# Kernel optimization log

Hardware: AMD Instinct MI355X
Metric: run time of the kernel (lower is better)

The kernel has to match this reference:

```python
import jax, jax.numpy as jnp
import numpy as np

N_HEAD = 8

def setup_inputs() -> dict:
    key = jax.random.key(0)
    ks = jax.random.split(key, 5)
    N, C, T, V = 64, 128, 64, 25
    x = jax.random.normal(ks[0], (N, C, T, V), dtype=jnp.float32)
    Wa = jax.random.normal(ks[1], (C, C), dtype=jnp.float32) * (1.0 / np.sqrt(C))
    ba = jax.random.normal(ks[2], (C,), dtype=jnp.float32) * 0.01
    Wp = jax.random.normal(ks[3], (C, C), dtype=jnp.float32) * (1.0 / np.sqrt(C))
    bp = jax.random.normal(ks[4], (C,), dtype=jnp.float32) * 0.01
    temp = jnp.ones((N_HEAD, 1), dtype=jnp.float32)
    denom_bias = jnp.zeros((N_HEAD, 1, 1), dtype=jnp.float32)
    return {"x": x, "Wa": Wa, "ba": ba, "Wp": Wp, "bp": bp, "temp": temp, "denom_bias": denom_bias}

def reference(x, Wa, ba, Wp, bp, temp, denom_bias):
    # x: (N, C, T, V); eval mode (dropout = identity); residual = identity (in==out, stride==1)
    N, C, T, V = x.shape
    H = N_HEAD
    hd = C // H
    res = x
    # 1x1 conv c_attn
    w = jnp.einsum('nctv,oc->notv', x, Wa) + ba[None, :, None, None]
    # (N,H,hd,T,V) -> (N,H,T,V,hd) -> (N,H,T*V,hd)
    w = w.reshape(N, H, hd, T, V).transpose(0, 1, 3, 4, 2).reshape(N, H, T * V, hd)
    w_sq = w * w
    denom = jnp.maximum(jnp.cumsum(w_sq, axis=2), 1e-12)
    w_normed = w_sq / denom + denom_bias  # denom_bias (H,1,1) broadcasts
    tmp = jnp.sum(w_normed, axis=-1) * temp  # (N,H,L) * (H,1)
    Pi = jax.nn.softmax(tmp, axis=2)  # (N,H,L)
    dots = jnp.cumsum(w_sq * Pi[..., None], axis=2) / (jnp.cumsum(Pi, axis=2) + 1e-8)[..., None]
    attn = 1.0 / (1.0 + dots)
    y = -(w * Pi[..., None]) * attn  # (N,H,L,hd)
    y = y.reshape(N, H, T, V, hd).transpose(0, 1, 4, 2, 3).reshape(N, C, T, V)
    y = jnp.einsum('nctv,oc->notv', y, Wp) + bp[None, :, None, None]
    y = y + res
    return jax.nn.relu(y)
```

## Files before the change

kernel.cpp:

```cpp
#include <hip/hip_runtime.h>
#include <hip/hip_bf16.h>

#define N_S     64
#define C_CH    128
#define L_SEQ   1600
#define H_HEADS 8
#define HD      16
#define SEGN    32
#define SEGL    50
#define PADW    136
#define PADT    70
#define NHQ     12800

typedef __attribute__((ext_vector_type(8))) short bf16x8;
typedef __attribute__((ext_vector_type(4))) float f32x4;

__device__ inline unsigned short f2bf(float f) {
  return __builtin_bit_cast(unsigned short, __float2bfloat16(f));
}
__device__ inline float bflo(unsigned int u) { return __builtin_bit_cast(float, u << 16); }
__device__ inline float bfhi(unsigned int u) { return __builtin_bit_cast(float, u & 0xffff0000u); }
__device__ inline unsigned int pk(float a, float b) {
  return (unsigned int)f2bf(a) | ((unsigned int)f2bf(b) << 16);
}

template <int CTRL>
__device__ inline float dppadd(float x) {
  int r = __builtin_amdgcn_update_dpp(0, __builtin_bit_cast(int, x), CTRL, 0xF, 0xF, true);
  return x + __builtin_bit_cast(float, r);
}


__global__ __launch_bounds__(256) void k_gemm1(const float* __restrict__ x,
                                               const float* __restrict__ Wa,
                                               const float* __restrict__ ba,
                                               unsigned int* __restrict__ w3) {
  __shared__ unsigned short was[128 * PADW];
  __shared__ unsigned short xs[128 * PADT];
  const int n = blockIdx.y;
  const int l0 = blockIdx.x * 64;
  const int t = threadIdx.x;
  const float* xn = x + (size_t)n * (C_CH * L_SEQ);

#pragma unroll
  for (int it = 0; it < 16; ++it) {
    int pos = it * 256 + t;
    int o = pos >> 5;
    int c4 = (pos & 31) << 2;
    float4 v = *reinterpret_cast<const float4*>(Wa + o * C_CH + c4);
    ushort4 u;
    u.x = f2bf(v.x); u.y = f2bf(v.y); u.z = f2bf(v.z); u.w = f2bf(v.w);
    *reinterpret_cast<ushort4*>(&was[o * PADW + c4]) = u;
  }
#pragma unroll
  for (int it = 0; it < 8; ++it) {
    int pos = it * 256 + t;
    int c = pos >> 4;
    int l4 = (pos & 15) << 2;
    float4 v = *reinterpret_cast<const float4*>(xn + (size_t)c * L_SEQ + l0 + l4);
    ushort4 u;
    u.x = f2bf(v.x); u.y = f2bf(v.y); u.z = f2bf(v.z); u.w = f2bf(v.w);
    *reinterpret_cast<ushort4*>(&xs[c * PADT + l4]) = u;
  }
  __syncthreads();

  const int wv = t >> 6;
  const int lane = t & 63;
  const int r16 = lane & 15;
  const int kg = lane >> 4;
  f32x4 acc[8];
#pragma unroll
  for (int ot = 0; ot < 8; ++ot) acc[ot] = (f32x4){0.f, 0.f, 0.f, 0.f};

#pragma unroll
  for (int ks = 0; ks < 4; ++ks) {
    bf16x8 a;
#pragma unroll
    for (int j = 0; j < 8; ++j)
      a[j] = (short)xs[(ks * 32 + kg * 8 + j) * PADT + wv * 16 + r16];
#pragma unroll
    for (int ot = 0; ot < 8; ++ot) {
      bf16x8 b = *reinterpret_cast<const bf16x8*>(&was[(ot * 16 + r16) * PADW + ks * 32 + kg * 8]);
      acc[ot] = __builtin_amdgcn_mfma_f32_16x16x32_bf16(a, b, acc[ot], 0, 0, 0);
    }
  }
  const int lbase = l0 + wv * 16 + kg * 4;
  const unsigned int lp0 = (unsigned int)lbase >> 1;
  const unsigned int seg0 = lp0 / 25u;
  const unsigned int ii0 = lp0 - seg0 * 25u;
  const unsigned int seg1 = (ii0 == 24u) ? seg0 + 1u : seg0;
  const unsigned int ii1 = (ii0 == 24u) ? 0u : ii0 + 1u;
  const unsigned int off0 = ii0 * 512u + seg0 * 16u + (unsigned int)r16;
  const unsigned int off1 = ii1 * 512u + seg1 * 16u + (unsigned int)r16;
  unsigned int* w3n = w3 + (size_t)(n * H_HEADS) * NHQ;
#pragma unroll
  for (int ot = 0; ot < 8; ++ot) {
    float bav = ba[ot * 16 + r16];
    unsigned int* p = w3n + (size_t)ot * NHQ;
    p[off0] = pk(acc[ot][0] + bav, acc[ot][1] + bav);
    p[off1] = pk(acc[ot][2] + bav, acc[ot][3] + bav);
  }
}

__global__ __launch_bounds__(512) void k_scan(const unsigned int* __restrict__ w3,
                                              unsigned int* __restrict__ y3,
                                              const float* __restrict__ temp,
                                              const float* __restrict__ dbias) {
  __shared__ float stot[SEGN][17];
  __shared__ float red[8];

  const int nh = blockIdx.x;
  const int h = nh & 7;
  const int t = threadIdx.x;
  const int d = t & 15;
  const int lane = t & 63;
  const int wv = t >> 6;
  const int seg = t >> 4;
  const float tscale = temp[h];
  const float db16 = 16.f * dbias[h];
  const float M = fmaxf((16.f + db16) * tscale, db16 * tscale);

  unsigned int vp[25];
  const unsigned int* srcd = w3 + (size_t)nh * NHQ;
#pragma unroll
  for (int ii = 0; ii < 25; ++ii) vp[ii] = srcd[ii * 512 + t];

  float tot = 0.f;
#pragma unroll
  for (int ii = 0; ii < 25; ++ii) {
    float a = bflo(vp[ii]), b = bfhi(vp[ii]);
    tot += a * a + b * b;
  }
  stot[seg][d] = tot;
  __syncthreads();
#pragma unroll
  for (int it = 0; it < 2; ++it) {
    int col = wv + it * 8;
    float val = (lane < 32) ? stot[lane][col] : 0.f;
#pragma unroll
    for (int sh = 1; sh < 32; sh <<= 1) {
      float nv = __shfl_up(val, sh);
      if (lane >= sh) val += nv;
    }
    if (lane < 32) stot[lane][col] = val;
  }
  __syncthreads();
  const float off = stot[seg][d] - tot;

  unsigned int ep[25];
  float run = off;
  float sAcc = 0.f, wpAcc = 0.f;
  float eprev = 0.f;
#pragma unroll
  for (int i = 0; i < SEGL; ++i) {
    float v = (i & 1) ? bfhi(vp[i >> 1]) : bflo(vp[i >> 1]);
    float wsq = v * v;
    run += wsq;
    float c = __fdividef(wsq, fmaxf(run, 1e-12f));
    c = dppadd<0x128>(c);
    c = dppadd<0x124>(c);
    c = dppadd<0x122>(c);
    c = dppadd<0x121>(c);
    float e = __expf((c + db16) * tscale - M);
    sAcc += e;
    wpAcc = fmaf(wsq, e, wpAcc);
    if (i & 1) ep[i >> 1] = pk(eprev, e); else eprev = e;
  }
  {
    float s = sAcc;
#pragma unroll
    for (int mask = 32; mask; mask >>= 1) s += __shfl_xor(s, mask);
    if (lane == 0) red[wv] = s;
  }
  __syncthreads();
  float S16 = 0.f;
#pragma unroll
  for (int i2 = 0; i2 < 8; ++i2) S16 += red[i2];
  const float S = S16 * 0.0625f;
  const float ninvS = -1.0f / S;
  const float epsS = 1e-8f * S;

  stot[seg][d] = wpAcc;
  if (d == 0) stot[seg][16] = sAcc;
  __syncthreads();
#pragma unroll
  for (int it = 0; it < 2; ++it) {
    int col = wv + it * 8;
    float val = (lane < 32) ? stot[lane][col] : 0.f;
#pragma unroll
    for (int sh = 1; sh < 32; sh <<= 1) {
      float nv = __shfl_up(val, sh);
      if (lane >= sh) val += nv;
    }
    if (lane < 32) stot[lane][col] = val;
  }
  if (wv == 0) {
    float val = (lane < 32) ? stot[lane][16] : 0.f;
#pragma unroll
    for (int sh = 1; sh < 32; sh <<= 1) {
      float nv = __shfl_up(val, sh);
      if (lane >= sh) val += nv;
    }
    if (lane < 32) stot[lane][16] = val;
  }
  __syncthreads();
  const float wp_off = stot[seg][d] - wpAcc;
  const float pi_off = stot[seg][16] - sAcc;

  {
    float run_wp = wp_off, run_pi = pi_off;
    float ylo = 0.f;
#pragma unroll
    for (int i = 0; i < SEGL; ++i) {
      float v = (i & 1) ? bfhi(vp[i >> 1]) : bflo(vp[i >> 1]);
      float e = (i & 1) ? bfhi(ep[i >> 1]) : bflo(ep[i >> 1]);
      run_pi += e;
      run_wp = fmaf(v * v, e, run_wp);
      float dn = run_pi + epsS;
      float y = (v * e) * __fdividef(dn, dn + run_wp) * ninvS;
      if (i & 1) vp[i >> 1] = pk(ylo, y); else ylo = y;
    }
  }
  unsigned int* dstd = y3 + (size_t)nh * NHQ;
#pragma unroll
  for (int ii = 0; ii < 25; ++ii) dstd[ii * 512 + t] = vp[ii];
}

__global__ __launch_bounds__(256) void k_gemm2(const unsigned int* __restrict__ y3,
                                               const float* __restrict__ Wp,
                                               const float* __restrict__ bp,
                                               const float* __restrict__ x,
                                               float* __restrict__ out) {
  __shared__ unsigned short wps[128 * PADW];
  __shared__ unsigned short ys[128 * PADT];
  const int n = blockIdx.y;
  const int l0 = blockIdx.x * 64;
  const int t = threadIdx.x;

#pragma unroll
  for (int it = 0; it < 16; ++it) {
    int pos = it * 256 + t;
    int o = pos >> 5;
    int c4 = (pos & 31) << 2;
    float4 v = *reinterpret_cast<const float4*>(Wp + o * C_CH + c4);
    ushort4 u;
    u.x = f2bf(v.x); u.y = f2bf(v.y); u.z = f2bf(v.z); u.w = f2bf(v.w);
    *reinterpret_cast<ushort4*>(&wps[o * PADW + c4]) = u;
  }
  const int lpb = l0 >> 1;
#pragma unroll
  for (int k = 0; k < 16; ++k) {
    int e = k * 256 + t;
    int lpl = e >> 7;
    int hd = e & 127;
    unsigned int lp = (unsigned int)(lpb + lpl);
    unsigned int sg = lp / 25u;
    unsigned int ii = lp - sg * 25u;
    unsigned int vdw = y3[(size_t)(n * H_HEADS + (hd >> 4)) * NHQ + ii * 512u + sg * 16u + (hd & 15)];
    *reinterpret_cast<unsigned int*>(&ys[hd * PADT + 2 * lpl]) = vdw;
  }
  __syncthreads();

  const int wv = t >> 6;
  const int lane = t & 63;
  const int r16 = lane & 15;
  const int kg = lane >> 4;
  f32x4 acc[8];
#pragma unroll
  for (int ot = 0; ot < 8; ++ot) acc[ot] = (f32x4){0.f, 0.f, 0.f, 0.f};

#pragma unroll
  for (int ks = 0; ks < 4; ++ks) {
    bf16x8 b;
#pragma unroll
    for (int j = 0; j < 8; ++j)
      b[j] = (short)ys[(ks * 32 + kg * 8 + j) * PADT + wv * 16 + r16];
#pragma unroll
    for (int ot = 0; ot < 8; ++ot) {
      bf16x8 a = *reinterpret_cast<const bf16x8*>(&wps[(ot * 16 + r16) * PADW + ks * 32 + kg * 8]);
      acc[ot] = __builtin_amdgcn_mfma_f32_16x16x32_bf16(a, b, acc[ot], 0, 0, 0);
    }
  }
  const int gl = l0 + wv * 16 + r16;
#pragma unroll
  for (int ot = 0; ot < 8; ++ot) {
#pragma unroll
    for (int i = 0; i < 4; ++i) {
      int o = ot * 16 + kg * 4 + i;
      size_t idx = (size_t)n * (C_CH * L_SEQ) + (size_t)o * L_SEQ + gl;
      float r = acc[ot][i] + bp[o] + x[idx];
      out[idx] = fmaxf(r, 0.f);
    }
  }
}

extern "C" void kernel_launch(void* const* d_in, const int* in_sizes, int n_in,
                              void* d_out, int out_size, void* d_ws, size_t ws_size,
                              hipStream_t stream) {
  const float* x     = (const float*)d_in[0];
  const float* Wa    = (const float*)d_in[1];
  const float* ba    = (const float*)d_in[2];
  const float* Wp    = (const float*)d_in[3];
  const float* bp    = (const float*)d_in[4];
  const float* temp  = (const float*)d_in[5];
  const float* dbias = (const float*)d_in[6];
  float* out = (float*)d_out;

  unsigned int* w3 = (unsigned int*)d_ws;
  unsigned int* y3 = w3 + (size_t)N_S * H_HEADS * NHQ;

  k_gemm1<<<dim3(L_SEQ / 64, N_S), 256, 0, stream>>>(x, Wa, ba, w3);
  k_scan<<<N_S * H_HEADS, 512, 0, stream>>>(w3, y3, temp, dbias);
  k_gemm2<<<dim3(L_SEQ / 64, N_S), 256, 0, stream>>>(y3, Wp, bp, x, out);
}
```

Before: 74.70 us.

## Store scan output in channel-major layout for vectorized gemm2 loads

```diff
diff --git a/kernel.cpp b/kernel.cpp
--- a/kernel.cpp
+++ b/kernel.cpp
@@ -9,7 +9,7 @@
 #define SEGN    32
 #define SEGL    50
 #define PADW    136
-#define PADT    70
+#define PADT    72
 #define NHQ     12800
 
 typedef __attribute__((ext_vector_type(8))) short bf16x8;
@@ -103,7 +103,7 @@
 }
 
 __global__ __launch_bounds__(512) void k_scan(const unsigned int* __restrict__ w3,
-                                              unsigned int* __restrict__ y3,
+                                              unsigned short* __restrict__ y2,
                                               const float* __restrict__ temp,
                                               const float* __restrict__ dbias) {
   __shared__ float stot[SEGN][17];
@@ -119,6 +119,8 @@
   const float tscale = temp[h];
   const float db16 = 16.f * dbias[h];
   const float M = fmaxf((16.f + db16) * tscale, db16 * tscale);
+  const float A = tscale * 1.44269504088896f;
+  const float B = (db16 * tscale - M) * 1.44269504088896f;
 
   unsigned int vp[25];
   const unsigned int* srcd = w3 + (size_t)nh * NHQ;
@@ -161,7 +163,7 @@
     c = dppadd<0x124>(c);
     c = dppadd<0x122>(c);
     c = dppadd<0x121>(c);
-    float e = __expf((c + db16) * tscale - M);
+    float e = exp2f(fmaf(c, A, B));
     sAcc += e;
     wpAcc = fmaf(wsq, e, wpAcc);
     if (i & 1) ep[i >> 1] = pk(eprev, e); else eprev = e;
@@ -221,12 +223,12 @@
       if (i & 1) vp[i >> 1] = pk(ylo, y); else ylo = y;
     }
   }
-  unsigned int* dstd = y3 + (size_t)nh * NHQ;
-#pragma unroll
-  for (int ii = 0; ii < 25; ++ii) dstd[ii * 512 + t] = vp[ii];
-}
-
-__global__ __launch_bounds__(256) void k_gemm2(const unsigned int* __restrict__ y3,
+  unsigned int* dstd = reinterpret_cast<unsigned int*>(y2) + ((size_t)nh * HD + d) * 800 + seg * 25;
+#pragma unroll
+  for (int ii = 0; ii < 25; ++ii) dstd[ii] = vp[ii];
+}
+
+__global__ __launch_bounds__(256) void k_gemm2(const unsigned short* __restrict__ y2,
                                                const float* __restrict__ Wp,
                                                const float* __restrict__ bp,
                                                const float* __restrict__ x,
@@ -247,17 +249,13 @@
     u.x = f2bf(v.x); u.y = f2bf(v.y); u.z = f2bf(v.z); u.w = f2bf(v.w);
     *reinterpret_cast<ushort4*>(&wps[o * PADW + c4]) = u;
   }
-  const int lpb = l0 >> 1;
-#pragma unroll
-  for (int k = 0; k < 16; ++k) {
-    int e = k * 256 + t;
-    int lpl = e >> 7;
-    int hd = e & 127;
-    unsigned int lp = (unsigned int)(lpb + lpl);
-    unsigned int sg = lp / 25u;
-    unsigned int ii = lp - sg * 25u;
-    unsigned int vdw = y3[(size_t)(n * H_HEADS + (hd >> 4)) * NHQ + ii * 512u + sg * 16u + (hd & 15)];
-    *reinterpret_cast<unsigned int*>(&ys[hd * PADT + 2 * lpl]) = vdw;
+#pragma unroll
+  for (int it = 0; it < 4; ++it) {
+    int pos = it * 256 + t;
+    int c = pos >> 3;
+    int l8 = (pos & 7) << 3;
+    uint4 v = *reinterpret_cast<const uint4*>(y2 + ((size_t)n * C_CH + c) * L_SEQ + l0 + l8);
+    *reinterpret_cast<uint4*>(&ys[c * PADT + l8]) = v;
   }
   __syncthreads();
 
@@ -307,9 +305,9 @@
   float* out = (float*)d_out;
 
   unsigned int* w3 = (unsigned int*)d_ws;
-  unsigned int* y3 = w3 + (size_t)N_S * H_HEADS * NHQ;
+  unsigned short* y2 = (unsigned short*)(w3 + (size_t)N_S * H_HEADS * NHQ);
 
   k_gemm1<<<dim3(L_SEQ / 64, N_S), 256, 0, stream>>>(x, Wa, ba, w3);
-  k_scan<<<N_S * H_HEADS, 512, 0, stream>>>(w3, y3, temp, dbias);
-  k_gemm2<<<dim3(L_SEQ / 64, N_S), 256, 0, stream>>>(y3, Wp, bp, x, out);
-}
+  k_scan<<<N_S * H_HEADS, 512, 0, stream>>>(w3, y2, temp, dbias);
+  k_gemm2<<<dim3(L_SEQ / 64, N_S), 256, 0, stream>>>(y2, Wp, bp, x, out);
+}
```

After: 75.12 us. Within noise of the previous version (+0.6%).
